# Kernel tuning notes

Hardware: AMD Instinct MI355X
Metric: run time of the kernel (lower is better)

## Reference

```python
import jax, jax.numpy as jnp
import numpy as np

B, NSL, DS = 8, 12, 768
L, R, DL = 24, 64, 4096
DP = 4096
DIM_T = NSL * 2 * DS          # 18432
FUSED = 1024 + 512            # 1536
GEN_IN = FUSED + 256 + 64     # 1856


def setup_inputs() -> dict:
    key = jax.random.key(0)
    ks = jax.random.split(key, 16)
    s = lambda d: 1.0 / np.sqrt(d)
    return {
        "A_small": jax.random.normal(ks[0], (B, NSL, 1, DS), jnp.float32),
        "B_small": jax.random.normal(ks[1], (B, NSL, DS, 1), jnp.float32),
        "prompt_emb": jax.random.normal(ks[2], (B, DP), jnp.float32),
        "W_ct": jax.random.normal(ks[3], (DIM_T, 1024), jnp.float32) * s(DIM_T),
        "b_ct": jnp.zeros((1024,), jnp.float32),
        "W_cp": jax.random.normal(ks[4], (DP, 512), jnp.float32) * s(DP),
        "b_cp": jnp.zeros((512,), jnp.float32),
        "W_pc": jax.random.normal(ks[5], (FUSED, L), jnp.float32) * s(FUSED),
        "b_pc": jnp.zeros((L,), jnp.float32),
        "E_layer": jax.random.normal(ks[6], (L, 256), jnp.float32),
        "E_chunk": jax.random.normal(ks[7], (R, 64), jnp.float32),
        "W_A": jax.random.normal(ks[8], (GEN_IN, DL), jnp.float32) * s(GEN_IN),
        "b_A": jnp.zeros((DL,), jnp.float32),
        "W_B": jax.random.normal(ks[9], (GEN_IN, DL), jnp.float32) * s(GEN_IN),
        "b_B": jnp.zeros((DL,), jnp.float32),
    }


def reference(A_small, B_small, prompt_emb, W_ct, b_ct, W_cp, b_cp, W_pc, b_pc,
              E_layer, E_chunk, W_A, b_A, W_B, b_B):
    bsz = prompt_emb.shape[0]
    flat_T = jnp.concatenate([A_small.reshape(bsz, -1), B_small.reshape(bsz, -1)], axis=-1)
    t_feat = jax.nn.relu(flat_T @ W_ct + b_ct)          # [B,1024]
    p_feat = jax.nn.relu(prompt_emb @ W_cp + b_cp)      # [B,512]
    fused = jnp.concatenate([t_feat, p_feat], axis=-1)  # [B,1536]
    logits = fused @ W_pc + b_pc                        # [B,L]
    y_soft = jax.nn.sigmoid(logits)                     # eval mode (no gumbel)
    y_hard = (y_soft > 0.5).astype(y_soft.dtype)
    gate = y_soft + jax.lax.stop_gradient(y_hard - y_soft)  # straight-through

    # Batched hypernetwork over all (layer, chunk) pairs instead of a double loop.
    ctx = jnp.broadcast_to(fused[:, None, None, :], (bsz, L, R, FUSED))
    le = jnp.broadcast_to(E_layer[None, :, None, :], (bsz, L, R, 256))
    ce = jnp.broadcast_to(E_chunk[None, None, :, :], (bsz, L, R, 64))
    gen = jnp.concatenate([ctx, le, ce], axis=-1)       # [B,L,R,1856]

    A = gen @ W_A + b_A                                 # [B,L,R,DL]
    Bm = gen @ W_B + b_B                                # [B,L,R,DL]
    A_large = A * gate[:, :, None, None]                # [B,L,R,DL]
    B_large = jnp.transpose(Bm, (0, 1, 3, 2))           # [B,L,DL,R]
    return (A_large, B_large, gate)
```

## Files before the change

kernel.cpp:

```cpp
#include <hip/hip_runtime.h>

typedef float v4f __attribute__((ext_vector_type(4)));

#define NB 8
#define NL 24
#define NR 64
#define ND 4096
#define NFUSED 1536
#define NTF 1024
#define NPF 512
#define KP 4096

#define TKC 144
#define PKC 32
#define FKC 12

#define WS_GATE  12288
#define WS_PLA   12480
#define WS_PLB   209088
#define WS_CA    405696
#define WS_CBT   667840
#define WS_PT    929984
#define WS_PP    2109632
#define WS_PFA   2240704
#define WS_PFB   2633920

__global__ __launch_bounds__(256) void k_indep(
    const float* __restrict__ As, const float* __restrict__ Bs,
    const float* __restrict__ W_ct,
    const float* __restrict__ prompt, const float* __restrict__ W_cp,
    const float* __restrict__ E_layer, const float* __restrict__ E_chunk,
    const float* __restrict__ W_A, const float* __restrict__ W_B,
    float* __restrict__ partT, float* __restrict__ partP,
    float* __restrict__ pLA, float* __restrict__ pLB,
    float* __restrict__ CA, float* __restrict__ CBT) {
  __shared__ float e[NR * 64];
  const int bx = blockIdx.x;
  const int tid = threadIdx.x;

  if (bx < 576) {
    const int j = (bx & 3) * 256 + tid;
    const int kc = bx >> 2;
    const int kbase = kc * 128;
    float acc[NB] = {};
    for (int kk = 0; kk < 128; ++kk) {
      const int k = kbase + kk;
      const float w = W_ct[(size_t)k * NTF + j];
      const float* x = (k < 9216) ? (As + k) : (Bs + (k - 9216));
#pragma unroll
      for (int b = 0; b < NB; ++b) acc[b] = fmaf(x[b * 9216], w, acc[b]);
    }
#pragma unroll
    for (int b = 0; b < NB; ++b)
      partT[(size_t)(kc * NB + b) * NTF + j] = acc[b];
  } else if (bx < 640) {
    const int t = bx - 576;
    const int j = (t & 1) * 256 + tid;
    const int kc = t >> 1;
    const int kbase = kc * 128;
    float acc[NB] = {};
    for (int kk = 0; kk < 128; ++kk) {
      const int k = kbase + kk;
      const float w = W_cp[(size_t)k * NPF + j];
#pragma unroll
      for (int b = 0; b < NB; ++b) acc[b] = fmaf(prompt[b * KP + k], w, acc[b]);
    }
#pragma unroll
    for (int b = 0; b < NB; ++b)
      partP[(size_t)(kc * NB + b) * NPF + j] = acc[b];
  } else if (bx < 704) {
    const int t = bx - 640;
    const bool isA = t < 32;
    const int tt = isA ? t : t - 32;
    const int dc = tt & 15;
    const int kh = tt >> 4;
    const float* W = (isA ? W_A : W_B) + (size_t)(NFUSED + kh * 128) * ND;
    float* pL = (isA ? pLA : pLB) + (size_t)kh * NL * ND;
    const int d = dc * 256 + tid;
    float acc[NL] = {};
    for (int kk = 0; kk < 128; ++kk) {
      const float w = W[(size_t)kk * ND + d];
      const float* el = E_layer + kh * 128 + kk;
#pragma unroll
      for (int l = 0; l < NL; ++l) acc[l] = fmaf(el[l * 256], w, acc[l]);
    }
#pragma unroll
    for (int l = 0; l < NL; ++l) pL[(size_t)l * ND + d] = acc[l];
  } else {
    const int t = bx - 704;
    const bool isA = t < 16;
    const int tt = isA ? t : t - 16;
    const float* W = (isA ? W_A : W_B) + (size_t)(NFUSED + 256) * ND;
    for (int i = tid; i < NR * 64; i += 256) e[i] = E_chunk[i];
    __syncthreads();
    const int d = tt * 256 + tid;
    float w[64];
#pragma unroll
    for (int k = 0; k < 64; ++k) w[k] = W[(size_t)k * ND + d];
    for (int r = 0; r < NR; ++r) {
      float s = 0.f;
#pragma unroll
      for (int k = 0; k < 64; ++k) s = fmaf(e[r * 64 + k], w[k], s);
      if (isA) CA[(size_t)r * ND + d] = s;
      else     CBT[(size_t)d * NR + r] = s;
    }
  }
}

__global__ __launch_bounds__(256) void k_dep(
    const float* __restrict__ partT, const float* __restrict__ partP,
    const float* __restrict__ b_ct, const float* __restrict__ b_cp,
    const float* __restrict__ W_A, const float* __restrict__ W_B,
    const float* __restrict__ W_pc, const float* __restrict__ b_pc,
    float* __restrict__ pFA, float* __restrict__ pFB,
    float* __restrict__ gate_ws, float* __restrict__ gate_out) {
  __shared__ float smem[1664];
  const int bx = blockIdx.x;
  const int tid = threadIdx.x;

  if (bx < 384) {
    const bool isA = bx < 192;
    const int t = isA ? bx : bx - 192;
    const float* W = isA ? W_A : W_B;
    float* part = isA ? pFA : pFB;
    const int dc = t & 15;
    const int kc = t >> 4;

    const int j = tid & 127;
    const int bhalf = tid >> 7;
    if (kc < 8) {
      const int gj = kc * 128 + j;
      const float bias = b_ct[gj];
#pragma unroll
      for (int p4 = 0; p4 < 4; ++p4) {
        const int b = p4 * 2 + bhalf;
        float s = bias;
        for (int kcc = 0; kcc < TKC; ++kcc)
          s += partT[(size_t)(kcc * NB + b) * NTF + gj];
        smem[b * 128 + j] = fmaxf(s, 0.f);
      }
    } else {
      const int jj = kc * 128 - NTF + j;
      const float bias = b_cp[jj];
#pragma unroll
      for (int p4 = 0; p4 < 4; ++p4) {
        const int b = p4 * 2 + bhalf;
        float s = bias;
        for (int kcc = 0; kcc < PKC; ++kcc)
          s += partP[(size_t)(kcc * NB + b) * NPF + jj];
        smem[b * 128 + j] = fmaxf(s, 0.f);
      }
    }
    __syncthreads();

    const int d = dc * 256 + tid;
    float acc[NB] = {};
    for (int kk = 0; kk < 128; ++kk) {
      const float w = W[(size_t)(kc * 128 + kk) * ND + d];
#pragma unroll
      for (int b = 0; b < NB; ++b) acc[b] = fmaf(smem[b * 128 + kk], w, acc[b]);
    }
#pragma unroll
    for (int b = 0; b < NB; ++b)
      part[(size_t)(kc * NB + b) * ND + d] = acc[b];
  } else {
    const int b = bx - 384;
    for (int j = tid; j < NFUSED; j += 256) {
      float s;
      if (j < NTF) {
        s = b_ct[j];
        for (int kc = 0; kc < TKC; ++kc)
          s += partT[(size_t)(kc * NB + b) * NTF + j];
      } else {
        const int jj = j - NTF;
        s = b_cp[jj];
        for (int kc = 0; kc < PKC; ++kc)
          s += partP[(size_t)(kc * NB + b) * NPF + jj];
      }
      smem[j] = fmaxf(s, 0.f);
    }
    __syncthreads();
    float acc[NL] = {};
    for (int j = tid; j < NFUSED; j += 256) {
      const float f = smem[j];
#pragma unroll
      for (int l = 0; l < NL; ++l) acc[l] = fmaf(f, W_pc[j * NL + l], acc[l]);
    }
#pragma unroll
    for (int off = 32; off > 0; off >>= 1)
#pragma unroll
      for (int l = 0; l < NL; ++l) acc[l] += __shfl_down(acc[l], off);
    const int wave = tid >> 6, lane = tid & 63;
    if (lane == 0)
#pragma unroll
      for (int l = 0; l < NL; ++l) smem[NFUSED + wave * NL + l] = acc[l];
    __syncthreads();
    if (tid < NL) {
      float s = b_pc[tid];
#pragma unroll
      for (int w = 0; w < 4; ++w) s += smem[NFUSED + w * NL + tid];
      const float g = s > 0.f ? 1.f : 0.f;
      gate_ws[b * NL + tid] = g;
      gate_out[b * NL + tid] = g;
    }
  }
}

__global__ __launch_bounds__(256) void k_out(
    const float* __restrict__ pFA, const float* __restrict__ pFB,
    const float* __restrict__ b_A, const float* __restrict__ b_B,
    const float* __restrict__ pLA, const float* __restrict__ pLB,
    const float* __restrict__ CA, const float* __restrict__ CBT,
    const float* __restrict__ gate,
    float* __restrict__ outA, float* __restrict__ outB) {
  __shared__ float sbase[512];
  const int bx = blockIdx.x;
  const int tid = threadIdx.x;
  if (bx < 1536) {
    const int bl = bx >> 3;
    const int rest = bx & 7;
    const int b = bl / NL, l = bl % NL;
    const int d = (rest >> 1) * 1024 + tid * 4;
    const int r0 = (rest & 1) * 32;
    const float g = gate[bl];
    v4f base = *(const v4f*)(b_A + d);
#pragma unroll
    for (int kc = 0; kc < FKC; ++kc)
      base += *(const v4f*)(pFA + (size_t)(kc * NB + b) * ND + d);
    base += *(const v4f*)(pLA + (size_t)l * ND + d);
    base += *(const v4f*)(pLA + (size_t)(NL + l) * ND + d);
    float* outp = outA + ((size_t)bl * NR + r0) * ND + d;
#pragma unroll 4
    for (int r = 0; r < 32; ++r) {
      const v4f c = *(const v4f*)(CA + (size_t)(r0 + r) * ND + d);
      const v4f v = (base + c) * g;
      __builtin_nontemporal_store(v, (v4f*)outp);
      outp += ND;
    }
  } else {
    const int t = bx - 1536;
    const int bl = t >> 3;
    const int b = bl / NL, l = bl % NL;
    const int dbase = (t & 7) * 512;
    for (int dd = tid; dd < 512; dd += 256) {
      const int d = dbase + dd;
      float s = b_B[d] + pLB[(size_t)l * ND + d] + pLB[(size_t)(NL + l) * ND + d];
#pragma unroll
      for (int kc = 0; kc < FKC; ++kc)
        s += pFB[(size_t)(kc * NB + b) * ND + d];
      sbase[dd] = s;
    }
    __syncthreads();
    const int dd16 = tid >> 4;
    const int r4 = (tid & 15) * 4;
#pragma unroll 4
    for (int i = 0; i < 32; ++i) {
      const int dloc = i * 16 + dd16;
      const int d = dbase + dloc;
      const v4f c = *(const v4f*)(CBT + (size_t)d * NR + r4);
      const v4f v = c + sbase[dloc];
      __builtin_nontemporal_store(v, (v4f*)(outB + ((size_t)bl * ND + d) * NR + r4));
    }
  }
}

extern "C" void kernel_launch(void* const* d_in, const int* in_sizes, int n_in,
                              void* d_out, int out_size, void* d_ws, size_t ws_size,
                              hipStream_t stream) {
  const float* A_small   = (const float*)d_in[0];
  const float* B_small   = (const float*)d_in[1];
  const float* prompt    = (const float*)d_in[2];
  const float* W_ct      = (const float*)d_in[3];
  const float* b_ct      = (const float*)d_in[4];
  const float* W_cp      = (const float*)d_in[5];
  const float* b_cp      = (const float*)d_in[6];
  const float* W_pc      = (const float*)d_in[7];
  const float* b_pc      = (const float*)d_in[8];
  const float* E_layer   = (const float*)d_in[9];
  const float* E_chunk   = (const float*)d_in[10];
  const float* W_A       = (const float*)d_in[11];
  const float* b_A       = (const float*)d_in[12];
  const float* W_B       = (const float*)d_in[13];
  const float* b_B       = (const float*)d_in[14];

  float* ws    = (float*)d_ws;
  float* gatew = ws + WS_GATE;
  float* pLA   = ws + WS_PLA;
  float* pLB   = ws + WS_PLB;
  float* CA    = ws + WS_CA;
  float* CBT   = ws + WS_CBT;
  float* partT = ws + WS_PT;
  float* partP = ws + WS_PP;
  float* pFA   = ws + WS_PFA;
  float* pFB   = ws + WS_PFB;

  float* outA = (float*)d_out;
  float* outB = outA + (size_t)192 * NR * ND;
  float* outG = outB + (size_t)192 * ND * NR;

  k_indep<<<736, 256, 0, stream>>>(A_small, B_small, W_ct, prompt, W_cp,
                                   E_layer, E_chunk, W_A, W_B,
                                   partT, partP, pLA, pLB, CA, CBT);
  k_dep<<<392, 256, 0, stream>>>(partT, partP, b_ct, b_cp, W_A, W_B,
                                 W_pc, b_pc, pFA, pFB, gatew, outG);
  k_out<<<3072, 256, 0, stream>>>(pFA, pFB, b_A, b_B, pLA, pLB, CA, CBT,
                                  gatew, outA, outB);
}
```

Measured before the change: 166.9 us.

## Add separate fused-feature reduction kernel and vectorize split-K GEMV stages

Adds a dedicated kernel that reduces the split-K partials of the context and prompt projections once into a fused feature buffer. Previously every k_dep block re-reduced those partials redundantly. The small GEMVs now stage activations in shared memory and load weights as float4, with finer K splits (more partials) and aliased workspace regions. The output kernel's block shapes also change: fewer, larger A-output blocks and a different B-transpose store pattern. The extra kernel launch and larger partial buffers are the added costs.

```diff
diff --git a/kernel.cpp b/kernel.cpp
--- a/kernel.cpp
+++ b/kernel.cpp
@@ -11,19 +11,20 @@
 #define NPF 512
 #define KP 4096
 
-#define TKC 144
-#define PKC 32
-#define FKC 12
-
+#define TKC 288
+#define PKC 128
+#define FKC 24
+
+#define WS_FUSED 0
 #define WS_GATE  12288
 #define WS_PLA   12480
 #define WS_PLB   209088
 #define WS_CA    405696
 #define WS_CBT   667840
 #define WS_PT    929984
-#define WS_PP    2109632
-#define WS_PFA   2240704
-#define WS_PFB   2633920
+#define WS_PP    3289280
+#define WS_PFA   929984
+#define WS_PFB   1716416
 
 __global__ __launch_bounds__(256) void k_indep(
     const float* __restrict__ As, const float* __restrict__ Bs,
@@ -34,42 +35,53 @@
     float* __restrict__ partT, float* __restrict__ partP,
     float* __restrict__ pLA, float* __restrict__ pLB,
     float* __restrict__ CA, float* __restrict__ CBT) {
-  __shared__ float e[NR * 64];
+  __shared__ float sm[4096];
   const int bx = blockIdx.x;
   const int tid = threadIdx.x;
 
-  if (bx < 576) {
-    const int j = (bx & 3) * 256 + tid;
-    const int kc = bx >> 2;
-    const int kbase = kc * 128;
-    float acc[NB] = {};
-    for (int kk = 0; kk < 128; ++kk) {
+  if (bx < 288) {
+    const int kc = bx;
+    const int kbase = kc * 64;
+    for (int i = tid; i < 512; i += 256) {
+      const int b = i >> 6, kk = i & 63;
       const int k = kbase + kk;
-      const float w = W_ct[(size_t)k * NTF + j];
-      const float* x = (k < 9216) ? (As + k) : (Bs + (k - 9216));
-#pragma unroll
-      for (int b = 0; b < NB; ++b) acc[b] = fmaf(x[b * 9216], w, acc[b]);
+      sm[i] = (k < 9216) ? As[b * 9216 + k] : Bs[b * 9216 + (k - 9216)];
+    }
+    __syncthreads();
+    const int c4 = tid * 4;
+    v4f acc[NB] = {};
+#pragma unroll 8
+    for (int kk = 0; kk < 64; ++kk) {
+      const v4f w = *(const v4f*)(W_ct + (size_t)(kbase + kk) * NTF + c4);
+#pragma unroll
+      for (int b = 0; b < NB; ++b) acc[b] += sm[b * 64 + kk] * w;
     }
 #pragma unroll
     for (int b = 0; b < NB; ++b)
-      partT[(size_t)(kc * NB + b) * NTF + j] = acc[b];
-  } else if (bx < 640) {
-    const int t = bx - 576;
-    const int j = (t & 1) * 256 + tid;
-    const int kc = t >> 1;
-    const int kbase = kc * 128;
-    float acc[NB] = {};
-    for (int kk = 0; kk < 128; ++kk) {
-      const int k = kbase + kk;
-      const float w = W_cp[(size_t)k * NPF + j];
-#pragma unroll
-      for (int b = 0; b < NB; ++b) acc[b] = fmaf(prompt[b * KP + k], w, acc[b]);
+      *(v4f*)(partT + (size_t)(kc * NB + b) * NTF + c4) = acc[b];
+  } else if (bx < 352) {
+    const int kc = bx - 288;
+    const int kbase = kc * 64;
+    for (int i = tid; i < 512; i += 256) {
+      const int b = i >> 6, kk = i & 63;
+      sm[i] = prompt[b * KP + kbase + kk];
+    }
+    __syncthreads();
+    const int p = tid >> 7;
+    const int c4 = (tid & 127) * 4;
+    v4f acc[NB] = {};
+#pragma unroll 8
+    for (int i = 0; i < 32; ++i) {
+      const int rr = 2 * i + p;
+      const v4f w = *(const v4f*)(W_cp + (size_t)(kbase + rr) * NPF + c4);
+#pragma unroll
+      for (int b = 0; b < NB; ++b) acc[b] += sm[b * 64 + rr] * w;
     }
 #pragma unroll
     for (int b = 0; b < NB; ++b)
-      partP[(size_t)(kc * NB + b) * NPF + j] = acc[b];
-  } else if (bx < 704) {
-    const int t = bx - 640;
+      *(v4f*)(partP + (size_t)((kc * 2 + p) * NB + b) * NPF + c4) = acc[b];
+  } else if (bx < 416) {
+    const int t = bx - 352;
     const bool isA = t < 32;
     const int tt = isA ? t : t - 32;
     const int dc = tt & 15;
@@ -87,11 +99,11 @@
 #pragma unroll
     for (int l = 0; l < NL; ++l) pL[(size_t)l * ND + d] = acc[l];
   } else {
-    const int t = bx - 704;
+    const int t = bx - 416;
     const bool isA = t < 16;
     const int tt = isA ? t : t - 16;
     const float* W = (isA ? W_A : W_B) + (size_t)(NFUSED + 256) * ND;
-    for (int i = tid; i < NR * 64; i += 256) e[i] = E_chunk[i];
+    for (int i = tid; i < NR * 64; i += 256) sm[i] = E_chunk[i];
     __syncthreads();
     const int d = tt * 256 + tid;
     float w[64];
@@ -100,89 +112,102 @@
     for (int r = 0; r < NR; ++r) {
       float s = 0.f;
 #pragma unroll
-      for (int k = 0; k < 64; ++k) s = fmaf(e[r * 64 + k], w[k], s);
+      for (int k = 0; k < 64; ++k) s = fmaf(sm[r * 64 + k], w[k], s);
       if (isA) CA[(size_t)r * ND + d] = s;
       else     CBT[(size_t)d * NR + r] = s;
     }
   }
 }
 
-__global__ __launch_bounds__(256) void k_dep(
+__global__ __launch_bounds__(256) void k_fused_reduce(
     const float* __restrict__ partT, const float* __restrict__ partP,
     const float* __restrict__ b_ct, const float* __restrict__ b_cp,
+    float* __restrict__ fused) {
+  __shared__ float red[256];
+  const int bx = blockIdx.x;
+  const int tid = threadIdx.x;
+  const int ks = tid >> 5, jl = tid & 31;
+  if (bx < 256) {
+    const int b = bx >> 5, jg = bx & 31;
+    const int j = jg * 32 + jl;
+    float s = 0.f;
+#pragma unroll 4
+    for (int t = 0; t < 36; ++t) {
+      const int kc = ks + 8 * t;
+      s += partT[(size_t)(kc * NB + b) * NTF + j];
+    }
+    red[tid] = s;
+    __syncthreads();
+    if (tid < 32) {
+      float tot = b_ct[j];
+#pragma unroll
+      for (int k = 0; k < 8; ++k) tot += red[k * 32 + tid];
+      fused[b * NFUSED + j] = fmaxf(tot, 0.f);
+    }
+  } else {
+    const int t0 = bx - 256;
+    const int b = t0 >> 4, jg = t0 & 15;
+    const int j = jg * 32 + jl;
+    float s = 0.f;
+#pragma unroll 4
+    for (int t = 0; t < 16; ++t) {
+      const int kc = ks + 8 * t;
+      s += partP[(size_t)(kc * NB + b) * NPF + j];
+    }
+    red[tid] = s;
+    __syncthreads();
+    if (tid < 32) {
+      float tot = b_cp[j];
+#pragma unroll
+      for (int k = 0; k < 8; ++k) tot += red[k * 32 + tid];
+      fused[b * NFUSED + NTF + j] = fmaxf(tot, 0.f);
+    }
+  }
+}
+
+__global__ __launch_bounds__(256) void k_dep(
+    const float* __restrict__ fused,
     const float* __restrict__ W_A, const float* __restrict__ W_B,
     const float* __restrict__ W_pc, const float* __restrict__ b_pc,
     float* __restrict__ pFA, float* __restrict__ pFB,
     float* __restrict__ gate_ws, float* __restrict__ gate_out) {
-  __shared__ float smem[1664];
+  __shared__ float sm[1664];
   const int bx = blockIdx.x;
   const int tid = threadIdx.x;
 
-  if (bx < 384) {
-    const bool isA = bx < 192;
-    const int t = isA ? bx : bx - 192;
-    const float* W = isA ? W_A : W_B;
-    float* part = isA ? pFA : pFB;
-    const int dc = t & 15;
-    const int kc = t >> 4;
-
-    const int j = tid & 127;
-    const int bhalf = tid >> 7;
-    if (kc < 8) {
-      const int gj = kc * 128 + j;
-      const float bias = b_ct[gj];
-#pragma unroll
-      for (int p4 = 0; p4 < 4; ++p4) {
-        const int b = p4 * 2 + bhalf;
-        float s = bias;
-        for (int kcc = 0; kcc < TKC; ++kcc)
-          s += partT[(size_t)(kcc * NB + b) * NTF + gj];
-        smem[b * 128 + j] = fmaxf(s, 0.f);
-      }
-    } else {
-      const int jj = kc * 128 - NTF + j;
-      const float bias = b_cp[jj];
-#pragma unroll
-      for (int p4 = 0; p4 < 4; ++p4) {
-        const int b = p4 * 2 + bhalf;
-        float s = bias;
-        for (int kcc = 0; kcc < PKC; ++kcc)
-          s += partP[(size_t)(kcc * NB + b) * NPF + jj];
-        smem[b * 128 + j] = fmaxf(s, 0.f);
-      }
-    }
-    __syncthreads();
-
-    const int d = dc * 256 + tid;
-    float acc[NB] = {};
-    for (int kk = 0; kk < 128; ++kk) {
-      const float w = W[(size_t)(kc * 128 + kk) * ND + d];
-#pragma unroll
-      for (int b = 0; b < NB; ++b) acc[b] = fmaf(smem[b * 128 + kk], w, acc[b]);
+  if (bx < 192) {
+    const bool isB = bx >= 96;
+    const int t = isB ? bx - 96 : bx;
+    const float* W = isB ? W_B : W_A;
+    float* pF = isB ? pFB : pFA;
+    const int cg = t & 7;
+    const int kc = t >> 3;
+    const int kbase = kc * 128;
+    for (int i = tid; i < 1024; i += 256) {
+      const int b = i >> 7, kk = i & 127;
+      sm[i] = fused[b * NFUSED + kbase + kk];
+    }
+    __syncthreads();
+    const int p = tid >> 7;
+    const int c4 = cg * 512 + (tid & 127) * 4;
+    v4f acc[NB] = {};
+#pragma unroll 8
+    for (int i = 0; i < 64; ++i) {
+      const int rr = 2 * i + p;
+      const v4f w = *(const v4f*)(W + (size_t)(kbase + rr) * ND + c4);
+#pragma unroll
+      for (int b = 0; b < NB; ++b) acc[b] += sm[b * 128 + rr] * w;
     }
 #pragma unroll
     for (int b = 0; b < NB; ++b)
-      part[(size_t)(kc * NB + b) * ND + d] = acc[b];
+      *(v4f*)(pF + (size_t)((kc * 2 + p) * NB + b) * ND + c4) = acc[b];
   } else {
-    const int b = bx - 384;
-    for (int j = tid; j < NFUSED; j += 256) {
-      float s;
-      if (j < NTF) {
-        s = b_ct[j];
-        for (int kc = 0; kc < TKC; ++kc)
-          s += partT[(size_t)(kc * NB + b) * NTF + j];
-      } else {
-        const int jj = j - NTF;
-        s = b_cp[jj];
-        for (int kc = 0; kc < PKC; ++kc)
-          s += partP[(size_t)(kc * NB + b) * NPF + jj];
-      }
-      smem[j] = fmaxf(s, 0.f);
-    }
+    const int b = bx - 192;
+    for (int j = tid; j < NFUSED; j += 256) sm[j] = fused[b * NFUSED + j];
     __syncthreads();
     float acc[NL] = {};
     for (int j = tid; j < NFUSED; j += 256) {
-      const float f = smem[j];
+      const float f = sm[j];
 #pragma unroll
       for (int l = 0; l < NL; ++l) acc[l] = fmaf(f, W_pc[j * NL + l], acc[l]);
     }
@@ -193,12 +218,12 @@
     const int wave = tid >> 6, lane = tid & 63;
     if (lane == 0)
 #pragma unroll
-      for (int l = 0; l < NL; ++l) smem[NFUSED + wave * NL + l] = acc[l];
+      for (int l = 0; l < NL; ++l) sm[NFUSED + wave * NL + l] = acc[l];
     __syncthreads();
     if (tid < NL) {
       float s = b_pc[tid];
 #pragma unroll
-      for (int w = 0; w < 4; ++w) s += smem[NFUSED + w * NL + tid];
+      for (int w = 0; w < 4; ++w) s += sm[NFUSED + w * NL + tid];
       const float g = s > 0.f ? 1.f : 0.f;
       gate_ws[b * NL + tid] = g;
       gate_out[b * NL + tid] = g;
@@ -216,12 +241,11 @@
   __shared__ float sbase[512];
   const int bx = blockIdx.x;
   const int tid = threadIdx.x;
-  if (bx < 1536) {
-    const int bl = bx >> 3;
-    const int rest = bx & 7;
+  if (bx < 768) {
+    const int bl = bx >> 2;
+    const int dg = bx & 3;
     const int b = bl / NL, l = bl % NL;
-    const int d = (rest >> 1) * 1024 + tid * 4;
-    const int r0 = (rest & 1) * 32;
+    const int d = dg * 1024 + tid * 4;
     const float g = gate[bl];
     v4f base = *(const v4f*)(b_A + d);
 #pragma unroll
@@ -229,16 +253,15 @@
       base += *(const v4f*)(pFA + (size_t)(kc * NB + b) * ND + d);
     base += *(const v4f*)(pLA + (size_t)l * ND + d);
     base += *(const v4f*)(pLA + (size_t)(NL + l) * ND + d);
-    float* outp = outA + ((size_t)bl * NR + r0) * ND + d;
+    float* outp = outA + (size_t)bl * NR * ND + d;
 #pragma unroll 4
-    for (int r = 0; r < 32; ++r) {
-      const v4f c = *(const v4f*)(CA + (size_t)(r0 + r) * ND + d);
+    for (int r = 0; r < NR; ++r) {
+      const v4f c = *(const v4f*)(CA + (size_t)r * ND + d);
       const v4f v = (base + c) * g;
-      __builtin_nontemporal_store(v, (v4f*)outp);
-      outp += ND;
+      __builtin_nontemporal_store(v, (v4f*)(outp + (size_t)r * ND));
     }
   } else {
-    const int t = bx - 1536;
+    const int t = bx - 768;
     const int bl = t >> 3;
     const int b = bl / NL, l = bl % NL;
     const int dbase = (t & 7) * 512;
@@ -251,15 +274,19 @@
       sbase[dd] = s;
     }
     __syncthreads();
-    const int dd16 = tid >> 4;
-    const int r4 = (tid & 15) * 4;
-#pragma unroll 4
-    for (int i = 0; i < 32; ++i) {
-      const int dloc = i * 16 + dd16;
+    const int dloc0 = tid >> 2;
+    const int r0 = (tid & 3) * 16;
+#pragma unroll 2
+    for (int i = 0; i < 8; ++i) {
+      const int dloc = i * 64 + dloc0;
       const int d = dbase + dloc;
-      const v4f c = *(const v4f*)(CBT + (size_t)d * NR + r4);
-      const v4f v = c + sbase[dloc];
-      __builtin_nontemporal_store(v, (v4f*)(outB + ((size_t)bl * ND + d) * NR + r4));
+      const float base = sbase[dloc];
+#pragma unroll
+      for (int q = 0; q < 4; ++q) {
+        const v4f c = *(const v4f*)(CBT + (size_t)d * NR + r0 + q * 4);
+        const v4f v = c + base;
+        __builtin_nontemporal_store(v, (v4f*)(outB + ((size_t)bl * ND + d) * NR + r0 + q * 4));
+      }
     }
   }
 }
@@ -284,6 +311,7 @@
   const float* b_B       = (const float*)d_in[14];
 
   float* ws    = (float*)d_ws;
+  float* fused = ws + WS_FUSED;
   float* gatew = ws + WS_GATE;
   float* pLA   = ws + WS_PLA;
   float* pLB   = ws + WS_PLB;
@@ -298,11 +326,12 @@
   float* outB = outA + (size_t)192 * NR * ND;
   float* outG = outB + (size_t)192 * ND * NR;
 
-  k_indep<<<736, 256, 0, stream>>>(A_small, B_small, W_ct, prompt, W_cp,
+  k_indep<<<448, 256, 0, stream>>>(A_small, B_small, W_ct, prompt, W_cp,
                                    E_layer, E_chunk, W_A, W_B,
                                    partT, partP, pLA, pLB, CA, CBT);
-  k_dep<<<392, 256, 0, stream>>>(partT, partP, b_ct, b_cp, W_A, W_B,
-                                 W_pc, b_pc, pFA, pFB, gatew, outG);
-  k_out<<<3072, 256, 0, stream>>>(pFA, pFB, b_A, b_B, pLA, pLB, CA, CBT,
+  k_fused_reduce<<<384, 256, 0, stream>>>(partT, partP, b_ct, b_cp, fused);
+  k_dep<<<200, 256, 0, stream>>>(fused, W_A, W_B, W_pc, b_pc,
+                                 pFA, pFB, gatew, outG);
+  k_out<<<2304, 256, 0, stream>>>(pFA, pFB, b_A, b_B, pLA, pLB, CA, CBT,
                                   gatew, outA, outB);
 }
```

Result: slower. 263.0 us (+57.6%).

## Replace split-K partial buffers with atomic accumulation into four replicas

Applied to the files above, without the earlier changes.

The split-K partial sums for the context and prompt projections are now atomically added into four replicated accumulators, instead of being written to large per-chunk partial buffers. The dependent kernel then sums only four replicas rather than looping over 144 or 32 partials, which removes a lot of redundant global reads. In exchange it adds an extra memset launch, atomic contention, and summation order that is no longer deterministic.

```diff
diff --git a/kernel.cpp b/kernel.cpp
--- a/kernel.cpp
+++ b/kernel.cpp
@@ -11,19 +11,16 @@
 #define NPF 512
 #define KP 4096
 
-#define TKC 144
-#define PKC 32
 #define FKC 12
 
-#define WS_GATE  12288
-#define WS_PLA   12480
-#define WS_PLB   209088
-#define WS_CA    405696
-#define WS_CBT   667840
-#define WS_PT    929984
-#define WS_PP    2109632
-#define WS_PFA   2240704
-#define WS_PFB   2633920
+#define WS_FACC  0
+#define WS_GATE  49152
+#define WS_PLA   49344
+#define WS_PLB   245952
+#define WS_CA    442560
+#define WS_CBT   704704
+#define WS_PFA   966848
+#define WS_PFB   1360064
 
 __global__ __launch_bounds__(256) void k_indep(
     const float* __restrict__ As, const float* __restrict__ Bs,
@@ -31,7 +28,7 @@
     const float* __restrict__ prompt, const float* __restrict__ W_cp,
     const float* __restrict__ E_layer, const float* __restrict__ E_chunk,
     const float* __restrict__ W_A, const float* __restrict__ W_B,
-    float* __restrict__ partT, float* __restrict__ partP,
+    float* __restrict__ fAcc,
     float* __restrict__ pLA, float* __restrict__ pLB,
     float* __restrict__ CA, float* __restrict__ CBT) {
   __shared__ float e[NR * 64];
@@ -50,9 +47,10 @@
 #pragma unroll
       for (int b = 0; b < NB; ++b) acc[b] = fmaf(x[b * 9216], w, acc[b]);
     }
+    const int rep = kc & 3;
 #pragma unroll
     for (int b = 0; b < NB; ++b)
-      partT[(size_t)(kc * NB + b) * NTF + j] = acc[b];
+      atomicAdd(fAcc + (size_t)(rep * NB + b) * NFUSED + j, acc[b]);
   } else if (bx < 640) {
     const int t = bx - 576;
     const int j = (t & 1) * 256 + tid;
@@ -65,9 +63,10 @@
 #pragma unroll
       for (int b = 0; b < NB; ++b) acc[b] = fmaf(prompt[b * KP + k], w, acc[b]);
     }
+    const int rep = kc & 3;
 #pragma unroll
     for (int b = 0; b < NB; ++b)
-      partP[(size_t)(kc * NB + b) * NPF + j] = acc[b];
+      atomicAdd(fAcc + (size_t)(rep * NB + b) * NFUSED + NTF + j, acc[b]);
   } else if (bx < 704) {
     const int t = bx - 640;
     const bool isA = t < 32;
@@ -108,13 +107,13 @@
 }
 
 __global__ __launch_bounds__(256) void k_dep(
-    const float* __restrict__ partT, const float* __restrict__ partP,
+    const float* __restrict__ fAcc,
     const float* __restrict__ b_ct, const float* __restrict__ b_cp,
     const float* __restrict__ W_A, const float* __restrict__ W_B,
     const float* __restrict__ W_pc, const float* __restrict__ b_pc,
     float* __restrict__ pFA, float* __restrict__ pFB,
     float* __restrict__ gate_ws, float* __restrict__ gate_out) {
-  __shared__ float smem[1664];
+  __shared__ float sm[1664];
   const int bx = blockIdx.x;
   const int tid = threadIdx.x;
 
@@ -125,40 +124,25 @@
     float* part = isA ? pFA : pFB;
     const int dc = t & 15;
     const int kc = t >> 4;
-
-    const int j = tid & 127;
-    const int bhalf = tid >> 7;
-    if (kc < 8) {
-      const int gj = kc * 128 + j;
-      const float bias = b_ct[gj];
-#pragma unroll
-      for (int p4 = 0; p4 < 4; ++p4) {
-        const int b = p4 * 2 + bhalf;
-        float s = bias;
-        for (int kcc = 0; kcc < TKC; ++kcc)
-          s += partT[(size_t)(kcc * NB + b) * NTF + gj];
-        smem[b * 128 + j] = fmaxf(s, 0.f);
-      }
-    } else {
-      const int jj = kc * 128 - NTF + j;
-      const float bias = b_cp[jj];
-#pragma unroll
-      for (int p4 = 0; p4 < 4; ++p4) {
-        const int b = p4 * 2 + bhalf;
-        float s = bias;
-        for (int kcc = 0; kcc < PKC; ++kcc)
-          s += partP[(size_t)(kcc * NB + b) * NPF + jj];
-        smem[b * 128 + j] = fmaxf(s, 0.f);
-      }
+    const int kbase = kc * 128;
+
+    for (int i = tid; i < 1024; i += 256) {
+      const int b = i >> 7, kk = i & 127;
+      const int k = kbase + kk;
+      float v = (k < NTF) ? b_ct[k] : b_cp[k - NTF];
+#pragma unroll
+      for (int rep = 0; rep < 4; ++rep)
+        v += fAcc[(size_t)(rep * NB + b) * NFUSED + k];
+      sm[i] = fmaxf(v, 0.f);
     }
     __syncthreads();
 
     const int d = dc * 256 + tid;
     float acc[NB] = {};
     for (int kk = 0; kk < 128; ++kk) {
-      const float w = W[(size_t)(kc * 128 + kk) * ND + d];
-#pragma unroll
-      for (int b = 0; b < NB; ++b) acc[b] = fmaf(smem[b * 128 + kk], w, acc[b]);
+      const float w = W[(size_t)(kbase + kk) * ND + d];
+#pragma unroll
+      for (int b = 0; b < NB; ++b) acc[b] = fmaf(sm[b * 128 + kk], w, acc[b]);
     }
 #pragma unroll
     for (int b = 0; b < NB; ++b)
@@ -166,23 +150,16 @@
   } else {
     const int b = bx - 384;
     for (int j = tid; j < NFUSED; j += 256) {
-      float s;
-      if (j < NTF) {
-        s = b_ct[j];
-        for (int kc = 0; kc < TKC; ++kc)
-          s += partT[(size_t)(kc * NB + b) * NTF + j];
-      } else {
-        const int jj = j - NTF;
-        s = b_cp[jj];
-        for (int kc = 0; kc < PKC; ++kc)
-          s += partP[(size_t)(kc * NB + b) * NPF + jj];
-      }
-      smem[j] = fmaxf(s, 0.f);
+      float v = (j < NTF) ? b_ct[j] : b_cp[j - NTF];
+#pragma unroll
+      for (int rep = 0; rep < 4; ++rep)
+        v += fAcc[(size_t)(rep * NB + b) * NFUSED + j];
+      sm[j] = fmaxf(v, 0.f);
     }
     __syncthreads();
     float acc[NL] = {};
     for (int j = tid; j < NFUSED; j += 256) {
-      const float f = smem[j];
+      const float f = sm[j];
 #pragma unroll
       for (int l = 0; l < NL; ++l) acc[l] = fmaf(f, W_pc[j * NL + l], acc[l]);
     }
@@ -193,12 +170,12 @@
     const int wave = tid >> 6, lane = tid & 63;
     if (lane == 0)
 #pragma unroll
-      for (int l = 0; l < NL; ++l) smem[NFUSED + wave * NL + l] = acc[l];
+      for (int l = 0; l < NL; ++l) sm[NFUSED + wave * NL + l] = acc[l];
     __syncthreads();
     if (tid < NL) {
       float s = b_pc[tid];
 #pragma unroll
-      for (int w = 0; w < 4; ++w) s += smem[NFUSED + w * NL + tid];
+      for (int w = 0; w < 4; ++w) s += sm[NFUSED + w * NL + tid];
       const float g = s > 0.f ? 1.f : 0.f;
       gate_ws[b * NL + tid] = g;
       gate_out[b * NL + tid] = g;
@@ -284,13 +261,12 @@
   const float* b_B       = (const float*)d_in[14];
 
   float* ws    = (float*)d_ws;
+  float* fAcc  = ws + WS_FACC;
   float* gatew = ws + WS_GATE;
   float* pLA   = ws + WS_PLA;
   float* pLB   = ws + WS_PLB;
   float* CA    = ws + WS_CA;
   float* CBT   = ws + WS_CBT;
-  float* partT = ws + WS_PT;
-  float* partP = ws + WS_PP;
   float* pFA   = ws + WS_PFA;
   float* pFB   = ws + WS_PFB;
 
@@ -298,10 +274,12 @@
   float* outB = outA + (size_t)192 * NR * ND;
   float* outG = outB + (size_t)192 * ND * NR;
 
+  hipMemsetAsync(fAcc, 0, (size_t)4 * NB * NFUSED * sizeof(float), stream);
+
   k_indep<<<736, 256, 0, stream>>>(A_small, B_small, W_ct, prompt, W_cp,
                                    E_layer, E_chunk, W_A, W_B,
-                                   partT, partP, pLA, pLB, CA, CBT);
-  k_dep<<<392, 256, 0, stream>>>(partT, partP, b_ct, b_cp, W_A, W_B,
+                                   fAcc, pLA, pLB, CA, CBT);
+  k_dep<<<392, 256, 0, stream>>>(fAcc, b_ct, b_cp, W_A, W_B,
                                  W_pc, b_pc, pFA, pFB, gatew, outG);
   k_out<<<3072, 256, 0, stream>>>(pFA, pFB, b_A, b_B, pLA, pLB, CA, CBT,
                                   gatew, outA, outB);
```

Result: faster. 142.8 us (-14.4%).
